# Kernel optimization log

Measured on AMD Instinct MI355X. Metric: run time of the kernel, lower is better.

## Reference

```python
import jax, jax.numpy as jnp
import numpy as np

HID = 4096
HEADS = 32
HEAD_DIM = 128
SEQ = 2048
GROUP = 128          # AWQ quantization group size along the input (K) dim
QKV_OUT = 3 * HID
ROPE_BASE = 10000.0


def dequant(qweight, scales, zeros):
    # qweight: [K, N] int; scales/zeros: [K//GROUP, N]
    s = jnp.repeat(scales, GROUP, axis=0)
    z = jnp.repeat(zeros, GROUP, axis=0)
    return (qweight.astype(jnp.float32) - z) * s


def rotate_half(x):
    x1, x2 = jnp.split(x, 2, axis=-1)
    return jnp.concatenate((-x2, x1), axis=-1)


def setup_inputs() -> dict:
    key = jax.random.key(0)
    ks = jax.random.split(key, 8)
    hidden_states = jax.random.normal(ks[0], (1, SEQ, HID), dtype=jnp.float32)
    position_ids = jnp.arange(SEQ, dtype=jnp.int32)[None, :]
    qkv_qweight = jax.random.randint(ks[1], (HID, QKV_OUT), 0, 16, dtype=jnp.int32)
    qkv_scales = jax.random.uniform(ks[2], (HID // GROUP, QKV_OUT), dtype=jnp.float32) * 0.002
    qkv_zeros = jax.random.uniform(ks[3], (HID // GROUP, QKV_OUT), dtype=jnp.float32) * 16.0
    o_qweight = jax.random.randint(ks[4], (HID, HID), 0, 16, dtype=jnp.int32)
    o_scales = jax.random.uniform(ks[5], (HID // GROUP, HID), dtype=jnp.float32) * 0.002
    o_zeros = jax.random.uniform(ks[6], (HID // GROUP, HID), dtype=jnp.float32) * 16.0
    return {"hidden_states": hidden_states, "position_ids": position_ids,
            "qkv_qweight": qkv_qweight, "qkv_scales": qkv_scales, "qkv_zeros": qkv_zeros,
            "o_qweight": o_qweight, "o_scales": o_scales, "o_zeros": o_zeros}


def reference(hidden_states, position_ids, qkv_qweight, qkv_scales, qkv_zeros,
              o_qweight, o_scales, o_zeros):
    b, s, _ = hidden_states.shape
    # --- quantized QKV projection (dequant + GEMM) ---
    w_qkv = dequant(qkv_qweight, qkv_scales, qkv_zeros)        # [HID, 3*HID]
    proj = jnp.einsum('bsk,kn->bsn', hidden_states, w_qkv)     # [b, s, 3*HID]
    xqkv = proj.reshape(b, s, 3, HEADS, HEAD_DIM)
    # [b, h, s, d]
    q = jnp.transpose(xqkv[:, :, 0], (0, 2, 1, 3))
    k = jnp.transpose(xqkv[:, :, 1], (0, 2, 1, 3))
    v = jnp.transpose(xqkv[:, :, 2], (0, 2, 1, 3))
    # --- rotary embedding (no KV cache: kv_seq_len == s) ---
    inv_freq = 1.0 / (ROPE_BASE ** (jnp.arange(0, HEAD_DIM, 2, dtype=jnp.float32) / HEAD_DIM))
    t = jnp.arange(s, dtype=jnp.float32)
    freqs = jnp.outer(t, inv_freq)                             # [s, d/2]
    emb = jnp.concatenate((freqs, freqs), axis=-1)             # [s, d]
    cos = jnp.cos(emb)[position_ids][:, None]                  # [b, 1, s, d]
    sin = jnp.sin(emb)[position_ids][:, None]
    q = q * cos + rotate_half(q) * sin
    k = k * cos + rotate_half(k) * sin
    # --- causal attention (flash_attn_func, padding_mask=None branch) ---
    scale = 1.0 / jnp.sqrt(jnp.float32(HEAD_DIM))
    scores = jnp.einsum('bhqd,bhkd->bhqk', q, k) * scale       # [b, h, s, s]
    causal = jnp.tril(jnp.ones((s, s), dtype=bool))
    scores = jnp.where(causal, scores, jnp.float32(-1e30))
    probs = jax.nn.softmax(scores, axis=-1)
    attn = jnp.einsum('bhqk,bhkd->bhqd', probs, v)             # [b, h, s, d]
    attn = jnp.transpose(attn, (0, 2, 1, 3)).reshape(b, s, HID)
    # --- quantized output projection ---
    w_o = dequant(o_qweight, o_scales, o_zeros)                # [HID, HID]
    out = jnp.einsum('bsk,kn->bsn', attn, w_o)                 # [b, s, HID]
    return out
```

## Files before the change

kernel.cpp:

```cpp
#include <hip/hip_runtime.h>
#include <hip/hip_bf16.h>

#define S_LEN 2048
#define HID_DIM 4096
#define NH 32
#define HD 128
#define NQKV 12288

typedef _Float16 half2v __attribute__((ext_vector_type(2)));
typedef _Float16 half4v __attribute__((ext_vector_type(4)));
typedef _Float16 half8v __attribute__((ext_vector_type(8)));
typedef float f32x4 __attribute__((ext_vector_type(4)));

typedef const __attribute__((address_space(1))) unsigned int* gas_u32;
typedef __attribute__((address_space(3))) unsigned int* las_u32;

__device__ inline void g2lds16(const _Float16* g, _Float16* l) {
  __builtin_amdgcn_global_load_lds((gas_u32)g, (las_u32)l, 16, 0, 0);
}

__global__ __launch_bounds__(256) void dequant_w(const int* __restrict__ W,
                                                 const float* __restrict__ scal,
                                                 const float* __restrict__ zer,
                                                 _Float16* __restrict__ Wt, int K, int N) {
  __shared__ _Float16 lT[64 * 84];
  const int k0 = blockIdx.y * 64, n0 = blockIdx.x * 64;
  const int tid = threadIdx.x, c = tid & 63, rp = tid >> 6;
  const int g = k0 >> 7;
  const float sc = scal[(size_t)g * N + n0 + c];
  const float zp = zer[(size_t)g * N + n0 + c];
#pragma unroll
  for (int i = 0; i < 8; ++i) {
    const int k = i * 8 + rp * 2;
    const float q0 = (float)W[(size_t)(k0 + k) * N + n0 + c];
    const float q1 = (float)W[(size_t)(k0 + k + 1) * N + n0 + c];
    half2v p;
    p[0] = (_Float16)((q0 - zp) * sc);
    p[1] = (_Float16)((q1 - zp) * sc);
    *(half2v*)&lT[c * 84 + k] = p;
  }
  __syncthreads();
  const int kc = tid & 7, nr0 = tid >> 3;
#pragma unroll
  for (int i = 0; i < 2; ++i) {
    const int n = nr0 + 32 * i;
    union { half8v v8; half4v v4[2]; } u;
    u.v4[0] = *(const half4v*)&lT[n * 84 + kc * 8];
    u.v4[1] = *(const half4v*)&lT[n * 84 + kc * 8 + 4];
    *(half8v*)&Wt[(size_t)(n0 + n) * K + k0 + kc * 8] = u.v8;
  }
}

__global__ __launch_bounds__(256) void conv_a(const float* __restrict__ A, _Float16* __restrict__ Af) {
  const int i = blockIdx.x * 256 + threadIdx.x;
  const float4 t = ((const float4*)A)[i];
  half4v r;
  r[0] = (_Float16)t.x; r[1] = (_Float16)t.y; r[2] = (_Float16)t.z; r[3] = (_Float16)t.w;
  ((half4v*)Af)[i] = r;
}

__device__ inline void stage128x64(const _Float16* __restrict__ gp, int K,
                                   _Float16* lp, int wave, int stR, int stC) {
  g2lds16(gp + (size_t)(wave * 16 + stR) * K + stC, lp + (wave * 2) * 512);
  g2lds16(gp + (size_t)(wave * 16 + 8 + stR) * K + stC, lp + (wave * 2 + 1) * 512);
}

template <int NB, typename CT>
__global__ __launch_bounds__(512, 2) void gemm_4ph(const _Float16* __restrict__ A,
                                                   const _Float16* __restrict__ Bt,
                                                   CT* __restrict__ C, int M, int N, int K) {
  constexpr int NBH = NB / 2;
  __shared__ _Float16 sA[3][2][128 * 64];
  __shared__ _Float16 sB[2][NBH][128 * 64];

  const int tid = threadIdx.x;
  const int wave = tid >> 6, lane = tid & 63;
  const int quad = lane >> 4, l16 = lane & 15;
  const int wr = wave >> 2;
  const int wc = wave & 3;
  const int NT = K >> 6;

  const _Float16* Ab = A + (size_t)(blockIdx.y * 256) * K;
  const _Float16* Bb = Bt + (size_t)(blockIdx.x * (NB * 64)) * K;

  const int stR = lane >> 3;
  const int stC = ((lane & 7) ^ stR) << 3;
  const int fx = l16 & 7;
  const int bh = (NB == 4) ? (wc >> 1) : 0;
  const int brow0 = (NB == 4) ? ((wc & 1) * 64) : (wc * 32);

#define COFF(ks_) ((((ks_) * 4 + quad) ^ fx) << 3)
#define SYNC_MFMA()                                  \
  __builtin_amdgcn_s_barrier();                      \
  asm volatile("s_waitcnt lgkmcnt(0)" ::: "memory"); \
  __builtin_amdgcn_sched_barrier(0);
#define MFMA_Q(moff_, noff_, bfr_)                                                       \
  __builtin_amdgcn_s_setprio(1);                                                         \
  _Pragma("unroll") for (int mb = 0; mb < 4; ++mb)                                       \
  _Pragma("unroll") for (int nb = 0; nb < NBH; ++nb)                                     \
  _Pragma("unroll") for (int ks = 0; ks < 2; ++ks)                                       \
      acc[(moff_) + mb][(noff_) + nb] = __builtin_amdgcn_mfma_f32_16x16x32_f16(          \
          af[mb][ks], bfr_[nb][ks], acc[(moff_) + mb][(noff_) + nb], 0, 0, 0);           \
  __builtin_amdgcn_s_setprio(0);

  f32x4 acc[8][NB];
  const f32x4 zero4 = {0.f, 0.f, 0.f, 0.f};
#pragma unroll
  for (int m8 = 0; m8 < 8; ++m8)
#pragma unroll
    for (int nb = 0; nb < NB; ++nb) acc[m8][nb] = zero4;

  stage128x64(Bb, K, &sB[0][0][0], wave, stR, stC);
  if constexpr (NB == 4)
    stage128x64(Bb + (size_t)128 * K, K, &sB[0][1][0], wave, stR, stC);
  stage128x64(Ab, K, &sA[0][0][0], wave, stR, stC);
  stage128x64(Ab + (size_t)128 * K, K, &sA[0][1][0], wave, stR, stC);
  stage128x64(Ab + 64, K, &sA[1][0][0], wave, stR, stC);
  stage128x64(Ab + (size_t)128 * K + 64, K, &sA[1][1][0], wave, stR, stC);
  asm volatile("s_waitcnt vmcnt(4)" ::: "memory");
  __builtin_amdgcn_s_barrier();

  int bA = 0;
  for (int t = 0; t < NT; ++t) {
    const int bB = t & 1;
    const int bA2 = (bA + 2 >= 3) ? bA - 1 : bA + 2;
    half8v af[4][2], blo[NBH][2], bhi[NBH][2];

#pragma unroll
    for (int mb = 0; mb < 4; ++mb)
#pragma unroll
      for (int ks = 0; ks < 2; ++ks)
        af[mb][ks] = *(const half8v*)&sA[bA][wr][(mb * 16 + l16) * 64 + COFF(ks)];
#pragma unroll
    for (int nb = 0; nb < NBH; ++nb)
#pragma unroll
      for (int ks = 0; ks < 2; ++ks)
        blo[nb][ks] = *(const half8v*)&sB[bB][bh][(brow0 + nb * 16 + l16) * 64 + COFF(ks)];
    if (t + 1 < NT)
      stage128x64(Bb + (size_t)(t + 1) * 64, K, &sB[bB ^ 1][0][0], wave, stR, stC);
    SYNC_MFMA()
    MFMA_Q(0, 0, blo)

#pragma unroll
    for (int nb = 0; nb < NBH; ++nb)
#pragma unroll
      for (int ks = 0; ks < 2; ++ks)
        bhi[nb][ks] =
            *(const half8v*)&sB[bB][bh][(brow0 + (NBH + nb) * 16 + l16) * 64 + COFF(ks)];
    if constexpr (NB == 4) {
      if (t + 1 < NT)
        stage128x64(Bb + (size_t)128 * K + (size_t)(t + 1) * 64, K, &sB[bB ^ 1][1][0], wave,
                    stR, stC);
    }
    SYNC_MFMA()
    MFMA_Q(0, NBH, bhi)

#pragma unroll
    for (int mb = 0; mb < 4; ++mb)
#pragma unroll
      for (int ks = 0; ks < 2; ++ks)
        af[mb][ks] = *(const half8v*)&sA[bA][wr][((64 + mb * 16 + l16)) * 64 + COFF(ks)];
    if (t + 2 < NT)
      stage128x64(Ab + (size_t)(t + 2) * 64, K, &sA[bA2][0][0], wave, stR, stC);
    SYNC_MFMA()
    MFMA_Q(4, NBH, bhi)

    if (t + 2 < NT) {
      stage128x64(Ab + (size_t)128 * K + (size_t)(t + 2) * 64, K, &sA[bA2][1][0], wave, stR, stC);
      asm volatile("s_waitcnt vmcnt(4)" ::: "memory");
    } else {
      asm volatile("s_waitcnt vmcnt(0)" ::: "memory");
    }
    SYNC_MFMA()
    MFMA_Q(4, 0, blo)

    bA = (bA + 1 >= 3) ? 0 : bA + 1;
  }

  const int rbase = blockIdx.y * 256 + wr * 128 + quad * 4;
  const int cbase = blockIdx.x * (NB * 64) + wc * (NB * 16) + l16;
#pragma unroll
  for (int m8 = 0; m8 < 8; ++m8) {
    const int rowb = rbase + (m8 >> 2) * 64 + (m8 & 3) * 16;
#pragma unroll
    for (int nb = 0; nb < NB; ++nb)
#pragma unroll
      for (int i = 0; i < 4; ++i)
        C[(size_t)(rowb + i) * N + cbase + nb * 16] = (CT)acc[m8][nb][i];
  }
#undef COFF
#undef SYNC_MFMA
#undef MFMA_Q
}

__global__ __launch_bounds__(256) void rope_kernel(const _Float16* __restrict__ proj,
                                                   const int* __restrict__ pos,
                                                   _Float16* __restrict__ Q, _Float16* __restrict__ K,
                                                   _Float16* __restrict__ Vt) {
  const int h = blockIdx.x, sb = blockIdx.y;
  const int tid = threadIdx.x;
  const int s0 = sb * 64;

#pragma unroll
  for (int it = 0; it < 16; ++it) {
    const int idx = it * 256 + tid;
    const int sl = idx >> 6, j = idx & 63;
    const int s = s0 + sl;
    const float p = (float)pos[s];
    const float invrev = exp2f(-0.20762050593045455f * (float)j) * 0.15915494309189535f;
    const float rev = p * invrev;
    const float frac = rev - floorf(rev);
    const float sn = __builtin_amdgcn_sinf(frac);
    const float cs = __builtin_amdgcn_cosf(frac);
    const _Float16* rp = proj + (size_t)s * NQKV + h * HD;
    {
      const float x1 = (float)rp[j], x2 = (float)rp[j + 64];
      _Float16* qp = Q + ((size_t)h * S_LEN + s) * HD;
      qp[j] = (_Float16)(x1 * cs - x2 * sn);
      qp[j + 64] = (_Float16)(x2 * cs + x1 * sn);
    }
    {
      const float x1 = (float)rp[HID_DIM + j], x2 = (float)rp[HID_DIM + j + 64];
      _Float16* kp = K + ((size_t)h * S_LEN + s) * HD;
      kp[j] = (_Float16)(x1 * cs - x2 * sn);
      kp[j + 64] = (_Float16)(x2 * cs + x1 * sn);
    }
  }

  __shared__ _Float16 lV[64 * 132];
#pragma unroll
  for (int r = 0; r < 4; ++r) {
    const int cid = r * 256 + tid;
    const int sl = cid >> 4;
    const int d0 = (cid & 15) * 8;
    const _Float16* vp = proj + (size_t)(s0 + sl) * NQKV + 2 * HID_DIM + h * HD + d0;
    *(half4v*)&lV[sl * 132 + d0] = *(const half4v*)vp;
    *(half4v*)&lV[sl * 132 + d0 + 4] = *(const half4v*)(vp + 4);
  }
  __syncthreads();
#pragma unroll
  for (int it = 0; it < 32; ++it) {
    const int d = it * 4 + (tid >> 6);
    const int sl = tid & 63;
    Vt[((size_t)h * HD + d) * S_LEN + s0 + sl] = lV[sl * 132 + d];
  }
}

__global__ __launch_bounds__(256) void flash_attn(const _Float16* __restrict__ Q,
                                                  const _Float16* __restrict__ Km,
                                                  const _Float16* __restrict__ Vt,
                                                  _Float16* __restrict__ O) {
  __shared__ _Float16 lK[32 * 128];
  __shared__ _Float16 lV[128 * 32];
  __shared__ _Float16 lP[4][2][16 * 40];
  const int h = blockIdx.y;
  const int xb = blockIdx.x;
  const int qb = (xb & 1) ? (15 - (xb >> 1)) : (xb >> 1);
  const int tid = threadIdx.x;
  const int wave = tid >> 6, lane = tid & 63;
  const int quad = lane >> 4, l16 = lane & 15;
  const int q0w = qb * 128 + wave * 32;
  const float scale = 0.08838834764831845f;

  const _Float16* Qh = Q + (size_t)h * S_LEN * HD;
  const _Float16* Kh = Km + (size_t)h * S_LEN * HD;
  const _Float16* Vh = Vt + (size_t)h * HD * S_LEN;

  const int kRow0 = wave * 8 + (lane >> 4);
  const int kSlot = lane & 15;
  const int vRow0 = wave * 32 + (lane >> 2);
  const int vSlot = lane & 3;

  half8v qf[2][4];
#pragma unroll
  for (int r = 0; r < 2; ++r)
#pragma unroll
    for (int c = 0; c < 4; ++c)
      qf[r][c] = *(const half8v*)&Qh[(size_t)(q0w + r * 16 + l16) * HD + c * 32 + quad * 8];

  const f32x4 zero4 = {0.f, 0.f, 0.f, 0.f};
  f32x4 o[2][8];
  f32x4 lp[2];
#pragma unroll
  for (int r = 0; r < 2; ++r) {
    lp[r] = zero4;
#pragma unroll
    for (int c = 0; c < 8; ++c) o[r][c] = zero4;
  }

  const int ntiles = 4 * qb + 4;
  for (int kt = 0; kt < ntiles; ++kt) {
#pragma unroll
    for (int i = 0; i < 2; ++i) {
      const int row = kRow0 + i * 4;
      const int ck = kSlot ^ (row & 15);
      g2lds16(Kh + (size_t)(kt * 32 + row) * HD + ck * 8, &lK[(wave * 8 + i * 4) * 128]);
    }
#pragma unroll
    for (int i = 0; i < 2; ++i) {
      const int row = vRow0 + i * 16;
      const int cv = vSlot ^ ((row >> 1) & 3);
      g2lds16(Vh + (size_t)row * S_LEN + kt * 32 + cv * 8, &lV[(wave * 32 + i * 16) * 32]);
    }
    __syncthreads();

    half8v kf[2][4];
#pragma unroll
    for (int hf = 0; hf < 2; ++hf)
#pragma unroll
      for (int c = 0; c < 4; ++c) {
        const int slot = (c * 4 + quad) ^ l16;
        kf[hf][c] = *(const half8v*)&lK[(hf * 16 + l16) * 128 + slot * 8];
      }
    half8v vf[8];
#pragma unroll
    for (int c = 0; c < 8; ++c) {
      const int slot = quad ^ ((l16 >> 1) & 3);
      vf[c] = *(const half8v*)&lV[(c * 16 + l16) * 32 + slot * 8];
    }

    f32x4 s[2][2];
#pragma unroll
    for (int r = 0; r < 2; ++r)
#pragma unroll
      for (int hf = 0; hf < 2; ++hf) {
        s[r][hf] = zero4;
#pragma unroll
        for (int c = 0; c < 4; ++c)
          s[r][hf] = __builtin_amdgcn_mfma_f32_16x16x32_f16(qf[r][c], kf[hf][c], s[r][hf], 0, 0, 0);
      }

#pragma unroll
    for (int r = 0; r < 2; ++r) {
      float p0[4], p1[4];
#pragma unroll
      for (int i = 0; i < 4; ++i) {
        const int row = q0w + r * 16 + quad * 4 + i;
        const int col0 = kt * 32 + l16, col1 = col0 + 16;
        const float e0 = __expf(s[r][0][i] * scale);
        const float e1 = __expf(s[r][1][i] * scale);
        p0[i] = (col0 <= row) ? e0 : 0.f;
        p1[i] = (col1 <= row) ? e1 : 0.f;
        lp[r][i] += p0[i] + p1[i];
      }
      _Float16* pw = lP[wave][r];
#pragma unroll
      for (int i = 0; i < 4; ++i) {
        pw[(quad * 4 + i) * 40 + l16] = (_Float16)p0[i];
        pw[(quad * 4 + i) * 40 + l16 + 16] = (_Float16)p1[i];
      }
    }
    half8v pa[2];
#pragma unroll
    for (int r = 0; r < 2; ++r) pa[r] = *(half8v*)&lP[wave][r][l16 * 40 + quad * 8];

#pragma unroll
    for (int c = 0; c < 8; ++c)
#pragma unroll
      for (int r = 0; r < 2; ++r)
        o[r][c] = __builtin_amdgcn_mfma_f32_16x16x32_f16(pa[r], vf[c], o[r][c], 0, 0, 0);

    __syncthreads();
  }

#pragma unroll
  for (int r = 0; r < 2; ++r) {
    f32x4 ls = lp[r];
#pragma unroll
    for (int off = 1; off < 16; off <<= 1) {
#pragma unroll
      for (int i = 0; i < 4; ++i) ls[i] += __shfl_xor(ls[i], off);
    }
    f32x4 inv;
#pragma unroll
    for (int i = 0; i < 4; ++i) inv[i] = 1.f / ls[i];
#pragma unroll
    for (int c = 0; c < 8; ++c) {
#pragma unroll
      for (int i = 0; i < 4; ++i) {
        const int row = q0w + r * 16 + quad * 4 + i;
        O[(size_t)row * HID_DIM + h * HD + c * 16 + l16] = (_Float16)(o[r][c][i] * inv[i]);
      }
    }
  }
}

extern "C" void kernel_launch(void* const* d_in, const int* in_sizes, int n_in,
                              void* d_out, int out_size, void* d_ws, size_t ws_size,
                              hipStream_t stream) {
  const float* hidden = (const float*)d_in[0];
  const int* pos = (const int*)d_in[1];
  const int* qkv_w = (const int*)d_in[2];
  const float* qkv_s = (const float*)d_in[3];
  const float* qkv_z = (const float*)d_in[4];
  const int* o_w = (const int*)d_in[5];
  const float* o_s = (const float*)d_in[6];
  const float* o_z = (const float*)d_in[7];

  char* ws = (char*)d_ws;
  _Float16* Wt_qkv = (_Float16*)(ws + 0);
  _Float16* Qb = (_Float16*)(ws + 0);
  _Float16* Kb = (_Float16*)(ws + 16777216);
  _Float16* Vtb = (_Float16*)(ws + 33554432);
  _Float16* Af16 = (_Float16*)(ws + 100663296);
  _Float16* attn = (_Float16*)(ws + 100663296);
  _Float16* proj = (_Float16*)(ws + 117440512);
  _Float16* Wt_o = (_Float16*)(ws + 117440512);
  float* out = (float*)d_out;

  hipLaunchKernelGGL(dequant_w, dim3(192, 64), dim3(256), 0, stream,
                     qkv_w, qkv_s, qkv_z, Wt_qkv, 4096, 12288);
  hipLaunchKernelGGL(conv_a, dim3(8192), dim3(256), 0, stream, hidden, Af16);
  hipLaunchKernelGGL((gemm_4ph<4, _Float16>), dim3(48, 8), dim3(512), 0, stream,
                     Af16, Wt_qkv, proj, 2048, 12288, 4096);
  hipLaunchKernelGGL(rope_kernel, dim3(32, 32), dim3(256), 0, stream, proj, pos, Qb, Kb, Vtb);
  hipLaunchKernelGGL(dequant_w, dim3(64, 64), dim3(256), 0, stream,
                     o_w, o_s, o_z, Wt_o, 4096, 4096);
  hipLaunchKernelGGL(flash_attn, dim3(16, 32), dim3(256), 0, stream, Qb, Kb, Vtb, attn);
  hipLaunchKernelGGL((gemm_4ph<2, float>), dim3(32, 8), dim3(512), 0, stream,
                     attn, Wt_o, out, 2048, 4096, 4096);
}
```

Baseline: 778.1 us.

## Add 256x192-tile QKV GEMM and triple-buffer K/V loads in flash attention

Adds a new QKV projection GEMM kernel with 256x192 output tiles, giving a 64x8 grid (512 blocks) in place of the previous 48x8 grid. This is meant to fill the CUs more evenly across waves. Flash attention now triple-buffers K/V tiles in LDS and prefetches the next tile while computing the current one. It also drops the trailing __syncthreads in favour of one barrier per iteration. This raises LDS use per block, which may reduce occupancy.

```diff
diff --git a/kernel.cpp b/kernel.cpp
--- a/kernel.cpp
+++ b/kernel.cpp
@@ -63,6 +63,130 @@
                                    _Float16* lp, int wave, int stR, int stC) {
   g2lds16(gp + (size_t)(wave * 16 + stR) * K + stC, lp + (wave * 2) * 512);
   g2lds16(gp + (size_t)(wave * 16 + 8 + stR) * K + stC, lp + (wave * 2 + 1) * 512);
+}
+__device__ inline void stage64x64(const _Float16* __restrict__ gp, int K,
+                                  _Float16* lp, int wave, int stR, int stC) {
+  g2lds16(gp + (size_t)(wave * 8 + stR) * K + stC, lp + wave * 512);
+}
+
+__global__ __launch_bounds__(512, 2) void gemm_192(const _Float16* __restrict__ A,
+                                                   const _Float16* __restrict__ Bt,
+                                                   _Float16* __restrict__ C, int M, int N, int K) {
+  __shared__ _Float16 sA[3][2][128 * 64];
+  __shared__ _Float16 sB[2][192 * 64];
+
+  const int tid = threadIdx.x;
+  const int wave = tid >> 6, lane = tid & 63;
+  const int quad = lane >> 4, l16 = lane & 15;
+  const int wr = wave >> 2;
+  const int wc = wave & 3;
+  const int NT = K >> 6;
+
+  const _Float16* Ab = A + (size_t)(blockIdx.y * 256) * K;
+  const _Float16* Bb = Bt + (size_t)(blockIdx.x * 192) * K;
+
+  const int stR = lane >> 3;
+  const int stC = ((lane & 7) ^ stR) << 3;
+  const int fx = l16 & 7;
+
+#define COFF(ks_) ((((ks_) * 4 + quad) ^ fx) << 3)
+#define SYNC_MFMA()                                  \
+  __builtin_amdgcn_s_barrier();                      \
+  asm volatile("s_waitcnt lgkmcnt(0)" ::: "memory"); \
+  __builtin_amdgcn_sched_barrier(0);
+
+  f32x4 acc[8][3];
+  const f32x4 zero4 = {0.f, 0.f, 0.f, 0.f};
+#pragma unroll
+  for (int m8 = 0; m8 < 8; ++m8)
+#pragma unroll
+    for (int nb = 0; nb < 3; ++nb) acc[m8][nb] = zero4;
+
+#pragma unroll
+  for (int j = 0; j < 3; ++j)
+    stage64x64(Bb + (size_t)(j * 64) * K, K, &sB[0][j * 4096], wave, stR, stC);
+  stage128x64(Ab, K, &sA[0][0][0], wave, stR, stC);
+  stage128x64(Ab + (size_t)128 * K, K, &sA[0][1][0], wave, stR, stC);
+  stage128x64(Ab + 64, K, &sA[1][0][0], wave, stR, stC);
+  stage128x64(Ab + (size_t)128 * K + 64, K, &sA[1][1][0], wave, stR, stC);
+  asm volatile("s_waitcnt vmcnt(4)" ::: "memory");
+  __builtin_amdgcn_s_barrier();
+
+  int bA = 0;
+  for (int t = 0; t < NT; ++t) {
+    const int bB = t & 1;
+    const int bA2 = (bA + 2 >= 3) ? bA - 1 : bA + 2;
+    half8v af[4][2], bf[3][2];
+
+#pragma unroll
+    for (int mb = 0; mb < 4; ++mb)
+#pragma unroll
+      for (int ks = 0; ks < 2; ++ks)
+        af[mb][ks] = *(const half8v*)&sA[bA][wr][(mb * 16 + l16) * 64 + COFF(ks)];
+#pragma unroll
+    for (int nb = 0; nb < 3; ++nb)
+#pragma unroll
+      for (int ks = 0; ks < 2; ++ks)
+        bf[nb][ks] = *(const half8v*)&sB[bB][(wc * 48 + nb * 16 + l16) * 64 + COFF(ks)];
+    if (t + 1 < NT) {
+#pragma unroll
+      for (int j = 0; j < 3; ++j)
+        stage64x64(Bb + (size_t)(j * 64) * K + (size_t)(t + 1) * 64, K,
+                   &sB[bB ^ 1][j * 4096], wave, stR, stC);
+    }
+    SYNC_MFMA()
+    __builtin_amdgcn_s_setprio(1);
+#pragma unroll
+    for (int mb = 0; mb < 4; ++mb)
+#pragma unroll
+      for (int nb = 0; nb < 3; ++nb)
+#pragma unroll
+        for (int ks = 0; ks < 2; ++ks)
+          acc[mb][nb] =
+              __builtin_amdgcn_mfma_f32_16x16x32_f16(af[mb][ks], bf[nb][ks], acc[mb][nb], 0, 0, 0);
+    __builtin_amdgcn_s_setprio(0);
+
+#pragma unroll
+    for (int mb = 0; mb < 4; ++mb)
+#pragma unroll
+      for (int ks = 0; ks < 2; ++ks)
+        af[mb][ks] = *(const half8v*)&sA[bA][wr][(64 + mb * 16 + l16) * 64 + COFF(ks)];
+    if (t + 2 < NT) {
+      const _Float16* Ap = Ab + (size_t)(t + 2) * 64;
+      stage128x64(Ap, K, &sA[bA2][0][0], wave, stR, stC);
+      stage128x64(Ap + (size_t)128 * K, K, &sA[bA2][1][0], wave, stR, stC);
+      asm volatile("s_waitcnt vmcnt(4)" ::: "memory");
+    } else if (t + 1 < NT) {
+      asm volatile("s_waitcnt vmcnt(0)" ::: "memory");
+    }
+    SYNC_MFMA()
+    __builtin_amdgcn_s_setprio(1);
+#pragma unroll
+    for (int mb = 0; mb < 4; ++mb)
+#pragma unroll
+      for (int nb = 0; nb < 3; ++nb)
+#pragma unroll
+        for (int ks = 0; ks < 2; ++ks)
+          acc[4 + mb][nb] = __builtin_amdgcn_mfma_f32_16x16x32_f16(af[mb][ks], bf[nb][ks],
+                                                                   acc[4 + mb][nb], 0, 0, 0);
+    __builtin_amdgcn_s_setprio(0);
+
+    bA = (bA + 1 >= 3) ? 0 : bA + 1;
+  }
+
+  const int rbase = blockIdx.y * 256 + wr * 128 + quad * 4;
+  const int cbase = blockIdx.x * 192 + wc * 48 + l16;
+#pragma unroll
+  for (int m8 = 0; m8 < 8; ++m8) {
+    const int rowb = rbase + (m8 >> 2) * 64 + (m8 & 3) * 16;
+#pragma unroll
+    for (int nb = 0; nb < 3; ++nb)
+#pragma unroll
+      for (int i = 0; i < 4; ++i)
+        C[(size_t)(rowb + i) * N + cbase + nb * 16] = (_Float16)acc[m8][nb][i];
+  }
+#undef COFF
+#undef SYNC_MFMA
 }
 
 template <int NB, typename CT>
@@ -250,8 +374,8 @@
                                                   const _Float16* __restrict__ Km,
                                                   const _Float16* __restrict__ Vt,
                                                   _Float16* __restrict__ O) {
-  __shared__ _Float16 lK[32 * 128];
-  __shared__ _Float16 lV[128 * 32];
+  __shared__ _Float16 lK[3][32 * 128];
+  __shared__ _Float16 lV[3][128 * 32];
   __shared__ _Float16 lP[4][2][16 * 40];
   const int h = blockIdx.y;
   const int xb = blockIdx.x;
@@ -271,6 +395,21 @@
   const int vRow0 = wave * 32 + (lane >> 2);
   const int vSlot = lane & 3;
 
+  auto stage_kv = [&](int kt_, int buf_) {
+#pragma unroll
+    for (int i = 0; i < 2; ++i) {
+      const int row = kRow0 + i * 4;
+      const int ck = kSlot ^ (row & 15);
+      g2lds16(Kh + (size_t)(kt_ * 32 + row) * HD + ck * 8, &lK[buf_][(wave * 8 + i * 4) * 128]);
+    }
+#pragma unroll
+    for (int i = 0; i < 2; ++i) {
+      const int row = vRow0 + i * 16;
+      const int cv = vSlot ^ ((row >> 1) & 3);
+      g2lds16(Vh + (size_t)row * S_LEN + kt_ * 32 + cv * 8, &lV[buf_][(wave * 32 + i * 16) * 32]);
+    }
+  };
+
   half8v qf[2][4];
 #pragma unroll
   for (int r = 0; r < 2; ++r)
@@ -289,20 +428,18 @@
   }
 
   const int ntiles = 4 * qb + 4;
+  stage_kv(0, 0);
+
+  int cb = 0;
   for (int kt = 0; kt < ntiles; ++kt) {
-#pragma unroll
-    for (int i = 0; i < 2; ++i) {
-      const int row = kRow0 + i * 4;
-      const int ck = kSlot ^ (row & 15);
-      g2lds16(Kh + (size_t)(kt * 32 + row) * HD + ck * 8, &lK[(wave * 8 + i * 4) * 128]);
-    }
-#pragma unroll
-    for (int i = 0; i < 2; ++i) {
-      const int row = vRow0 + i * 16;
-      const int cv = vSlot ^ ((row >> 1) & 3);
-      g2lds16(Vh + (size_t)row * S_LEN + kt * 32 + cv * 8, &lV[(wave * 32 + i * 16) * 32]);
-    }
-    __syncthreads();
+    const int nb3 = (cb + 1 >= 3) ? 0 : cb + 1;
+    if (kt + 1 < ntiles) {
+      stage_kv(kt + 1, nb3);
+      asm volatile("s_waitcnt vmcnt(4)" ::: "memory");
+    } else {
+      asm volatile("s_waitcnt vmcnt(0)" ::: "memory");
+    }
+    __builtin_amdgcn_s_barrier();
 
     half8v kf[2][4];
 #pragma unroll
@@ -310,13 +447,13 @@
 #pragma unroll
       for (int c = 0; c < 4; ++c) {
         const int slot = (c * 4 + quad) ^ l16;
-        kf[hf][c] = *(const half8v*)&lK[(hf * 16 + l16) * 128 + slot * 8];
+        kf[hf][c] = *(const half8v*)&lK[cb][(hf * 16 + l16) * 128 + slot * 8];
       }
     half8v vf[8];
 #pragma unroll
     for (int c = 0; c < 8; ++c) {
       const int slot = quad ^ ((l16 >> 1) & 3);
-      vf[c] = *(const half8v*)&lV[(c * 16 + l16) * 32 + slot * 8];
+      vf[c] = *(const half8v*)&lV[cb][(c * 16 + l16) * 32 + slot * 8];
     }
 
     f32x4 s[2][2];
@@ -360,7 +497,7 @@
       for (int r = 0; r < 2; ++r)
         o[r][c] = __builtin_amdgcn_mfma_f32_16x16x32_f16(pa[r], vf[c], o[r][c], 0, 0, 0);
 
-    __syncthreads();
+    cb = nb3;
   }
 
 #pragma unroll
@@ -411,7 +548,7 @@
   hipLaunchKernelGGL(dequant_w, dim3(192, 64), dim3(256), 0, stream,
                      qkv_w, qkv_s, qkv_z, Wt_qkv, 4096, 12288);
   hipLaunchKernelGGL(conv_a, dim3(8192), dim3(256), 0, stream, hidden, Af16);
-  hipLaunchKernelGGL((gemm_4ph<4, _Float16>), dim3(48, 8), dim3(512), 0, stream,
+  hipLaunchKernelGGL(gemm_192, dim3(64, 8), dim3(512), 0, stream,
                      Af16, Wt_qkv, proj, 2048, 12288, 4096);
   hipLaunchKernelGGL(rope_kernel, dim3(32, 32), dim3(256), 0, stream, proj, pos, Qb, Kb, Vtb);
   hipLaunchKernelGGL(dequant_w, dim3(64, 64), dim3(256), 0, stream,
```

After: 740.5 us. 4.8% less time.
